# Kernel optimization log

Hardware: AMD Instinct MI355X
Metric: run time of the kernel (lower is better)

The kernel has to match this reference:

```python
import jax, jax.numpy as jnp
import numpy as np
import math

HEADS = 4
LN_EPS = 1e-5


def _layer_norm(x, gamma, beta):
    # LayerNorm over last dim (N=4096), matching nn.LayerNorm(4096)
    mu = jnp.mean(x, axis=-1, keepdims=True)
    var = jnp.mean((x - mu) ** 2, axis=-1, keepdims=True)
    return (x - mu) * jax.lax.rsqrt(var + LN_EPS) * gamma + beta


def setup_inputs() -> dict:
    key = jax.random.key(0)
    ks = jax.random.split(key, 10)
    L, IMG, N = 1024, 1024, 4096
    s_img = 1.0 / math.sqrt(IMG)
    s_L = 1.0 / math.sqrt(L)
    return {
        "point_features": jax.random.normal(ks[0], (1, L, N), jnp.float32),
        "img_features": jax.random.normal(ks[1], (1, IMG, N), jnp.float32),
        # 4 per-head 1x1 convs IMG_chl -> L_chl
        "W_img": jax.random.normal(ks[2], (HEADS, L, IMG), jnp.float32) * s_img,
        "b_img": jax.random.normal(ks[3], (HEADS, L), jnp.float32) * s_img,
        # conv_L: L_chl -> L_chl
        "W_L": jax.random.normal(ks[4], (L, L), jnp.float32) * s_L,
        "b_L": jax.random.normal(ks[5], (L,), jnp.float32) * s_L,
        # LayerNorm(4096)
        "ln_g": jnp.ones((N,), jnp.float32),
        "ln_b": jnp.zeros((N,), jnp.float32),
        # conv_fusion: L_chl -> L_chl
        "W_f": jax.random.normal(ks[6], (L, L), jnp.float32) * s_L,
        "b_f": jax.random.normal(ks[7], (L,), jnp.float32) * s_L,
    }


def reference(point_features, img_features, W_img, b_img, W_L, b_L, ln_g, ln_b, W_f, b_f):
    # L_query = conv_L(point_features): [1, L, N]
    L_query = jnp.einsum('oi,bin->bon', W_L, point_features) + b_L[None, :, None]
    dk = L_query.shape[1]
    N = L_query.shape[2]

    # All 4 head keys at once: [H, 1, L, N]
    keys = jnp.einsum('hoi,bin->hbon', W_img, img_features) + b_img[:, None, :, None]

    # score_i = sum_c(key_i * query) / sqrt(dk)  -> cat over heads: [H, N] (B=1)
    score = jnp.sum(keys * L_query[None], axis=2).reshape(HEADS, N) / jnp.sqrt(jnp.float32(dk))

    # softmax across heads (dim=0), weightmap = [1, H, N]
    weight = jax.nn.softmax(score, axis=0)
    weightmap = weight[None]

    # z = sum_h weight[h] * key_h : [1, L, N]
    z = jnp.einsum('hn,hbcn->bcn', weight, keys)

    fused = _layer_norm(z + L_query, ln_g, ln_b)
    fusion_features = jnp.einsum('oi,bin->bon', W_f, fused) + b_f[None, :, None]
    return (fusion_features, weightmap)
```

## Files before the change

### kernel.cpp

```cpp
#include <hip/hip_runtime.h>
#include <hip/hip_bf16.h>
#include <stdint.h>

using u16 = unsigned short;

typedef __attribute__((ext_vector_type(8))) short bf16x8;
typedef __attribute__((ext_vector_type(4))) float f32x4;

typedef const __attribute__((address_space(1))) unsigned int* gas_t;
typedef __attribute__((address_space(3))) unsigned int* las_t;

__device__ inline void g2l16(const u16* g, u16* l) {
  __builtin_amdgcn_global_load_lds((gas_t)g, (las_t)l, 16, 0, 0);
}

__device__ inline u16 f2b(float x) {
  union { float f; uint32_t u; } v; v.f = x;
  uint32_t r = (v.u + 0x7FFFu + ((v.u >> 16) & 1u)) >> 16;
  return (u16)r;
}
__device__ inline float b2f(u16 b) {
  union { uint32_t u; float f; } v; v.u = ((uint32_t)b) << 16;
  return v.f;
}

__device__ inline void store_out(float* p, float v) { *p = v; }
__device__ inline void store_out(u16* p, float v) { *p = f2b(v); }

template<typename OutT>
__global__ __launch_bounds__(256)
void gemm_bt(const u16* __restrict__ A, const u16* __restrict__ Bt,
             const float* __restrict__ bias, OutT* __restrict__ C,
             int M, int N, int K)
{
  __shared__ u16 As[128 * 64];
  __shared__ u16 Bs[128 * 64];

  const int tid  = threadIdx.x;
  const int wave = tid >> 6;
  const int lane = tid & 63;
  const int wm = wave >> 1, wn = wave & 1;
  const int lr = lane & 15;
  const int lq = lane >> 4;
  const int x7 = lr & 7;

  const int m0 = blockIdx.y * 128;
  const int n0 = blockIdx.x * 128;

  const int srow = tid >> 3;
  const int sgc  = (tid & 7) ^ (srow & 7);
  const u16* gA = A  + (size_t)(m0 + srow) * K + sgc * 8;
  const u16* gB = Bt + (size_t)(n0 + srow) * K + sgc * 8;
  u16* dstA = As + wave * 512;
  u16* dstB = Bs + wave * 512;

  f32x4 acc[4][4];
  #pragma unroll
  for (int i = 0; i < 4; ++i)
    #pragma unroll
    for (int j = 0; j < 4; ++j)
      acc[i][j] = (f32x4){0.f, 0.f, 0.f, 0.f};

  for (int k0 = 0; k0 < K; k0 += 64) {
    #pragma unroll
    for (int s = 0; s < 4; ++s) {
      g2l16(gA + (size_t)(s * 32) * K + k0, dstA + s * 2048);
      g2l16(gB + (size_t)(s * 32) * K + k0, dstB + s * 2048);
    }
    __syncthreads();

    #pragma unroll
    for (int ks = 0; ks < 2; ++ks) {
      const int pa = (ks * 4 + lq) ^ x7;
      bf16x8 af[4], bfr[4];
      #pragma unroll
      for (int im = 0; im < 4; ++im)
        af[im] = *(const bf16x8*)&As[(wm * 64 + im * 16 + lr) * 64 + pa * 8];
      #pragma unroll
      for (int in = 0; in < 4; ++in)
        bfr[in] = *(const bf16x8*)&Bs[(wn * 64 + in * 16 + lr) * 64 + pa * 8];

      #pragma unroll
      for (int im = 0; im < 4; ++im)
        #pragma unroll
        for (int in = 0; in < 4; ++in)
          acc[im][in] = __builtin_amdgcn_mfma_f32_16x16x32_bf16(
              af[im], bfr[in], acc[im][in], 0, 0, 0);
    }
    __syncthreads();
  }

  #pragma unroll
  for (int im = 0; im < 4; ++im) {
    const int mbase = m0 + wm * 64 + im * 16 + lq * 4;
    #pragma unroll
    for (int in = 0; in < 4; ++in) {
      const int ncol = n0 + wn * 64 + in * 16 + lr;
      #pragma unroll
      for (int r = 0; r < 4; ++r) {
        const int m = mbase + r;
        store_out(C + (size_t)m * N + ncol, acc[im][in][r] + bias[m]);
      }
    }
  }
}

template<typename OutT>
__global__ __launch_bounds__(256)
void gemm_bt_64(const u16* __restrict__ A, const u16* __restrict__ Bt,
                const float* __restrict__ bias, OutT* __restrict__ C,
                int M, int N, int K)
{
  __shared__ u16 As[64 * 64];
  __shared__ u16 Bs[128 * 64];

  const int tid  = threadIdx.x;
  const int wave = tid >> 6;
  const int lane = tid & 63;
  const int lr = lane & 15;
  const int lq = lane >> 4;
  const int x7 = lr & 7;

  const int m0 = blockIdx.y * 64;
  const int n0 = blockIdx.x * 128;

  const int srow = tid >> 3;
  const int sgc  = (tid & 7) ^ (srow & 7);
  const u16* gA = A  + (size_t)(m0 + srow) * K + sgc * 8;
  const u16* gB = Bt + (size_t)(n0 + srow) * K + sgc * 8;
  u16* dstA = As + wave * 512;
  u16* dstB = Bs + wave * 512;

  f32x4 acc[4][2];
  #pragma unroll
  for (int i = 0; i < 4; ++i)
    #pragma unroll
    for (int j = 0; j < 2; ++j)
      acc[i][j] = (f32x4){0.f, 0.f, 0.f, 0.f};

  for (int k0 = 0; k0 < K; k0 += 64) {
    #pragma unroll
    for (int s = 0; s < 2; ++s)
      g2l16(gA + (size_t)(s * 32) * K + k0, dstA + s * 2048);
    #pragma unroll
    for (int s = 0; s < 4; ++s)
      g2l16(gB + (size_t)(s * 32) * K + k0, dstB + s * 2048);
    __syncthreads();

    #pragma unroll
    for (int ks = 0; ks < 2; ++ks) {
      const int pa = (ks * 4 + lq) ^ x7;
      bf16x8 af[4], bfr[2];
      #pragma unroll
      for (int im = 0; im < 4; ++im)
        af[im] = *(const bf16x8*)&As[(im * 16 + lr) * 64 + pa * 8];
      #pragma unroll
      for (int in = 0; in < 2; ++in)
        bfr[in] = *(const bf16x8*)&Bs[(wave * 32 + in * 16 + lr) * 64 + pa * 8];

      #pragma unroll
      for (int im = 0; im < 4; ++im)
        #pragma unroll
        for (int in = 0; in < 2; ++in)
          acc[im][in] = __builtin_amdgcn_mfma_f32_16x16x32_bf16(
              af[im], bfr[in], acc[im][in], 0, 0, 0);
    }
    __syncthreads();
  }

  #pragma unroll
  for (int im = 0; im < 4; ++im) {
    const int mbase = m0 + im * 16 + lq * 4;
    #pragma unroll
    for (int in = 0; in < 2; ++in) {
      const int ncol = n0 + wave * 32 + in * 16 + lr;
      #pragma unroll
      for (int r = 0; r < 4; ++r) {
        const int m = mbase + r;
        store_out(C + (size_t)m * N + ncol, acc[im][in][r] + bias[m]);
      }
    }
  }
}

__global__ __launch_bounds__(256)
void cast_transpose2(const float* __restrict__ in0, u16* __restrict__ out0,
                     const float* __restrict__ in1, u16* __restrict__ out1,
                     int R, int C)
{
  const float* in = blockIdx.z ? in1 : in0;
  u16* out = blockIdx.z ? out1 : out0;
  __shared__ u16 tile[32][33];
  const int c0 = blockIdx.x * 32, r0 = blockIdx.y * 32;
  const int tx = threadIdx.x & 31, ty = threadIdx.x >> 5;
  #pragma unroll
  for (int k = 0; k < 4; ++k)
    tile[ty + 8 * k][tx] = f2b(in[(size_t)(r0 + ty + 8 * k) * C + c0 + tx]);
  __syncthreads();
  #pragma unroll
  for (int k = 0; k < 4; ++k)
    out[(size_t)(c0 + ty + 8 * k) * R + r0 + tx] = tile[tx][ty + 8 * k];
}

__global__ __launch_bounds__(256)
void transpose_u16(const u16* __restrict__ in, u16* __restrict__ out,
                   int R, int C)
{
  __shared__ u16 tile[32][33];
  const int c0 = blockIdx.x * 32, r0 = blockIdx.y * 32;
  const int tx = threadIdx.x & 31, ty = threadIdx.x >> 5;
  #pragma unroll
  for (int k = 0; k < 4; ++k)
    tile[ty + 8 * k][tx] = in[(size_t)(r0 + ty + 8 * k) * C + c0 + tx];
  __syncthreads();
  #pragma unroll
  for (int k = 0; k < 4; ++k)
    out[(size_t)(c0 + ty + 8 * k) * R + r0 + tx] = tile[tx][ty + 8 * k];
}

__global__ __launch_bounds__(256)
void cast_weights(const float4* __restrict__ wim, const float4* __restrict__ wl,
                  const float4* __restrict__ wf, ushort4* __restrict__ wimb,
                  ushort4* __restrict__ wlb, ushort4* __restrict__ wfb)
{
  int i = blockIdx.x * 256 + threadIdx.x;
  const float4* src; ushort4* dst;
  if (i < 1048576)      { src = wim; dst = wimb; }
  else if (i < 1310720) { src = wl;  dst = wlb;  i -= 1048576; }
  else                  { src = wf;  dst = wfb;  i -= 1310720; }
  const float4 v = src[i];
  ushort4 o;
  o.x = f2b(v.x); o.y = f2b(v.y); o.z = f2b(v.z); o.w = f2b(v.w);
  dst[i] = o;
}

__global__ __launch_bounds__(256)
void score_partial(const u16* __restrict__ keys, const float* __restrict__ Q,
                   float* __restrict__ spart)
{
  const int n  = blockIdx.x * 256 + threadIdx.x;
  const int cb = blockIdx.y;
  const int c0 = cb * 128;
  float s[4] = {0.f, 0.f, 0.f, 0.f};
  for (int c = c0; c < c0 + 128; ++c) {
    const float q = Q[(size_t)c * 4096 + n];
    #pragma unroll
    for (int h = 0; h < 4; ++h)
      s[h] = fmaf(q, b2f(keys[((size_t)((h << 10) + c)) * 4096 + n]), s[h]);
  }
  #pragma unroll
  for (int h = 0; h < 4; ++h)
    spart[((size_t)cb * 4 + h) * 4096 + n] = s[h];
}

__global__ __launch_bounds__(256)
void softmax_h(const float* __restrict__ spart, float* __restrict__ wmap)
{
  const int n = blockIdx.x * 256 + threadIdx.x;
  float s[4] = {0.f, 0.f, 0.f, 0.f};
  #pragma unroll
  for (int cb = 0; cb < 8; ++cb)
    #pragma unroll
    for (int h = 0; h < 4; ++h)
      s[h] += spart[((size_t)cb * 4 + h) * 4096 + n];
  #pragma unroll
  for (int h = 0; h < 4; ++h) s[h] *= 0.03125f;
  const float m = fmaxf(fmaxf(s[0], s[1]), fmaxf(s[2], s[3]));
  const float e0 = expf(s[0] - m), e1 = expf(s[1] - m);
  const float e2 = expf(s[2] - m), e3 = expf(s[3] - m);
  const float inv = 1.f / (e0 + e1 + e2 + e3);
  wmap[n] = e0 * inv; wmap[4096 + n] = e1 * inv;
  wmap[8192 + n] = e2 * inv; wmap[12288 + n] = e3 * inv;
}

__global__ __launch_bounds__(256)
void z_ln(const u16* __restrict__ keys, const float* __restrict__ Q,
          const float* __restrict__ w, const float* __restrict__ g,
          const float* __restrict__ bb, u16* __restrict__ fused)
{
  const int c  = blockIdx.x;
  const int tx = threadIdx.x;
  float t[16];
  float s = 0.f, s2 = 0.f;
  #pragma unroll
  for (int j = 0; j < 16; ++j) {
    const int n = tx + j * 256;
    const float q = Q[(size_t)c * 4096 + n];
    float z = 0.f;
    #pragma unroll
    for (int h = 0; h < 4; ++h)
      z = fmaf(w[h * 4096 + n], b2f(keys[((size_t)((h << 10) + c)) * 4096 + n]), z);
    const float v = z + q;
    t[j] = v; s += v; s2 = fmaf(v, v, s2);
  }
  #pragma unroll
  for (int o = 32; o > 0; o >>= 1) {
    s  += __shfl_down(s, o);
    s2 += __shfl_down(s2, o);
  }
  __shared__ float rbuf[8];
  const int wave = tx >> 6, lane = tx & 63;
  if (lane == 0) { rbuf[wave] = s; rbuf[4 + wave] = s2; }
  __syncthreads();
  s  = rbuf[0] + rbuf[1] + rbuf[2] + rbuf[3];
  s2 = rbuf[4] + rbuf[5] + rbuf[6] + rbuf[7];
  const float mu  = s * (1.f / 4096.f);
  const float var = s2 * (1.f / 4096.f) - mu * mu;
  const float rs  = rsqrtf(var + 1e-5f);
  #pragma unroll
  for (int j = 0; j < 16; ++j) {
    const int n = tx + j * 256;
    fused[(size_t)c * 4096 + n] = f2b((t[j] - mu) * rs * g[n] + bb[n]);
  }
}

extern "C" void kernel_launch(void* const* d_in, const int* in_sizes, int n_in,
                              void* d_out, int out_size, void* d_ws, size_t ws_size,
                              hipStream_t stream)
{
  const float* P   = (const float*)d_in[0];
  const float* I   = (const float*)d_in[1];
  const float* Wim = (const float*)d_in[2];
  const float* bim = (const float*)d_in[3];
  const float* WL  = (const float*)d_in[4];
  const float* bL  = (const float*)d_in[5];
  const float* lng = (const float*)d_in[6];
  const float* lnb = (const float*)d_in[7];
  const float* Wf  = (const float*)d_in[8];
  const float* bf_ = (const float*)d_in[9];
  float* out = (float*)d_out;

  char* ws = (char*)d_ws;
  u16*   PT     = (u16*)(ws + 0);
  u16*   IT     = (u16*)(ws + (size_t)8  * 1048576);
  u16*   WLb    = (u16*)(ws + (size_t)16 * 1048576);
  u16*   WIb    = (u16*)(ws + (size_t)18 * 1048576);
  u16*   WFb    = (u16*)(ws + (size_t)26 * 1048576);
  float* Q      = (float*)(ws + (size_t)28 * 1048576);
  u16*   KEYS   = (u16*)(ws + (size_t)44 * 1048576);
  float* SPART  = (float*)(ws + (size_t)76 * 1048576);
  u16*   FUSED  = (u16*)(ws + (size_t)77 * 1048576);
  u16*   FUSEDT = (u16*)(ws + (size_t)85 * 1048576);

  const dim3 b256(256);

  cast_transpose2<<<dim3(128, 32, 2), b256, 0, stream>>>(P, PT, I, IT, 1024, 4096);
  cast_weights<<<6144, b256, 0, stream>>>((const float4*)Wim, (const float4*)WL,
                                          (const float4*)Wf, (ushort4*)WIb,
                                          (ushort4*)WLb, (ushort4*)WFb);

  gemm_bt_64<float><<<dim3(32, 16), b256, 0, stream>>>(WLb, PT, bL, Q, 1024, 4096, 1024);
  gemm_bt<u16><<<dim3(32, 32), b256, 0, stream>>>(WIb, IT, bim, KEYS, 4096, 4096, 1024);

  score_partial<<<dim3(16, 8), b256, 0, stream>>>(KEYS, Q, SPART);
  float* wmap = out + (size_t)1024 * 4096;
  softmax_h<<<16, b256, 0, stream>>>(SPART, wmap);

  z_ln<<<1024, b256, 0, stream>>>(KEYS, Q, wmap, lng, lnb, FUSED);
  transpose_u16<<<dim3(128, 32), b256, 0, stream>>>(FUSED, FUSEDT, 1024, 4096);

  gemm_bt_64<float><<<dim3(32, 16), b256, 0, stream>>>(WFb, FUSEDT, bf_, out, 1024, 4096, 1024);
}
```

Measured before the change: 232.0 us.

## Merge prep kernels, fuse Q and keys GEMMs, store Q as bf16

Merges the input cast-transpose and weight-cast kernels into one prep launch. The Q projection and the four-head key projection now run in a single 128x128-tile GEMM launch with 1280 blocks instead of two launches, which removes a launch and a tail. Q is stored as bf16 rather than fp32, halving its write and read traffic in the score and LayerNorm stages. In exchange the residual L_query path loses precision, since it is rounded to bf16.

```diff
diff --git a/kernel.cpp b/kernel.cpp
--- a/kernel.cpp
+++ b/kernel.cpp
@@ -28,14 +28,13 @@
 __device__ inline void store_out(u16* p, float v) { *p = f2b(v); }
 
 template<typename OutT>
-__global__ __launch_bounds__(256)
-void gemm_bt(const u16* __restrict__ A, const u16* __restrict__ Bt,
-             const float* __restrict__ bias, OutT* __restrict__ C,
-             int M, int N, int K)
-{
-  __shared__ u16 As[128 * 64];
-  __shared__ u16 Bs[128 * 64];
-
+__device__ inline void gemm_tile_128(const u16* __restrict__ A,
+                                     const u16* __restrict__ Bt,
+                                     const float* __restrict__ bias,
+                                     OutT* __restrict__ C,
+                                     int m0, int n0, int N, int K,
+                                     u16* As, u16* Bs)
+{
   const int tid  = threadIdx.x;
   const int wave = tid >> 6;
   const int lane = tid & 63;
@@ -44,9 +43,6 @@
   const int lq = lane >> 4;
   const int x7 = lr & 7;
 
-  const int m0 = blockIdx.y * 128;
-  const int n0 = blockIdx.x * 128;
-
   const int srow = tid >> 3;
   const int sgc  = (tid & 7) ^ (srow & 7);
   const u16* gA = A  + (size_t)(m0 + srow) * K + sgc * 8;
@@ -105,6 +101,25 @@
   }
 }
 
+__global__ __launch_bounds__(256)
+void gemm_keys_q(const u16* __restrict__ WIb, const u16* __restrict__ IT,
+                 const float* __restrict__ bim, u16* __restrict__ KEYS,
+                 const u16* __restrict__ WLb, const u16* __restrict__ PT,
+                 const float* __restrict__ bL, u16* __restrict__ Qb)
+{
+  __shared__ u16 As[128 * 64];
+  __shared__ u16 Bs[128 * 64];
+  const int by = blockIdx.y;
+  const bool keys = (by < 32);
+  const u16*   A    = keys ? WIb : WLb;
+  const u16*   Bt   = keys ? IT  : PT;
+  const float* bias = keys ? bim : bL;
+  u16*         C    = keys ? KEYS : Qb;
+  const int m0 = (by & 31) * 128;
+  const int n0 = blockIdx.x * 128;
+  gemm_tile_128<u16>(A, Bt, bias, C, m0, n0, 4096, 1024, As, Bs);
+}
+
 template<typename OutT>
 __global__ __launch_bounds__(256)
 void gemm_bt_64(const u16* __restrict__ A, const u16* __restrict__ Bt,
@@ -184,18 +199,53 @@
 }
 
 __global__ __launch_bounds__(256)
-void cast_transpose2(const float* __restrict__ in0, u16* __restrict__ out0,
-                     const float* __restrict__ in1, u16* __restrict__ out1,
-                     int R, int C)
-{
-  const float* in = blockIdx.z ? in1 : in0;
-  u16* out = blockIdx.z ? out1 : out0;
+void prep(const float* __restrict__ P, u16* __restrict__ PT,
+          const float* __restrict__ I, u16* __restrict__ IT,
+          const float4* __restrict__ wim, const float4* __restrict__ wl,
+          const float4* __restrict__ wf, ushort4* __restrict__ wimb,
+          ushort4* __restrict__ wlb, ushort4* __restrict__ wfb)
+{
+  const int bid = blockIdx.x;
+  if (bid < 8192) {
+    const int z   = bid >> 12;
+    const int rem = bid & 4095;
+    const int bx  = rem & 127;
+    const int byy = rem >> 7;
+    const float* in = z ? I : P;
+    u16* out = z ? IT : PT;
+    __shared__ u16 tile[32][33];
+    const int c0 = bx * 32, r0 = byy * 32;
+    const int tx = threadIdx.x & 31, ty = threadIdx.x >> 5;
+    #pragma unroll
+    for (int k = 0; k < 4; ++k)
+      tile[ty + 8 * k][tx] = f2b(in[(size_t)(r0 + ty + 8 * k) * 4096 + c0 + tx]);
+    __syncthreads();
+    #pragma unroll
+    for (int k = 0; k < 4; ++k)
+      out[(size_t)(c0 + ty + 8 * k) * 1024 + r0 + tx] = tile[tx][ty + 8 * k];
+  } else {
+    int i = (bid - 8192) * 256 + threadIdx.x;
+    const float4* src; ushort4* dst;
+    if (i < 1048576)      { src = wim; dst = wimb; }
+    else if (i < 1310720) { src = wl;  dst = wlb;  i -= 1048576; }
+    else                  { src = wf;  dst = wfb;  i -= 1310720; }
+    const float4 v = src[i];
+    ushort4 o;
+    o.x = f2b(v.x); o.y = f2b(v.y); o.z = f2b(v.z); o.w = f2b(v.w);
+    dst[i] = o;
+  }
+}
+
+__global__ __launch_bounds__(256)
+void transpose_u16(const u16* __restrict__ in, u16* __restrict__ out,
+                   int R, int C)
+{
   __shared__ u16 tile[32][33];
   const int c0 = blockIdx.x * 32, r0 = blockIdx.y * 32;
   const int tx = threadIdx.x & 31, ty = threadIdx.x >> 5;
   #pragma unroll
   for (int k = 0; k < 4; ++k)
-    tile[ty + 8 * k][tx] = f2b(in[(size_t)(r0 + ty + 8 * k) * C + c0 + tx]);
+    tile[ty + 8 * k][tx] = in[(size_t)(r0 + ty + 8 * k) * C + c0 + tx];
   __syncthreads();
   #pragma unroll
   for (int k = 0; k < 4; ++k)
@@ -203,39 +253,7 @@
 }
 
 __global__ __launch_bounds__(256)
-void transpose_u16(const u16* __restrict__ in, u16* __restrict__ out,
-                   int R, int C)
-{
-  __shared__ u16 tile[32][33];
-  const int c0 = blockIdx.x * 32, r0 = blockIdx.y * 32;
-  const int tx = threadIdx.x & 31, ty = threadIdx.x >> 5;
-  #pragma unroll
-  for (int k = 0; k < 4; ++k)
-    tile[ty + 8 * k][tx] = in[(size_t)(r0 + ty + 8 * k) * C + c0 + tx];
-  __syncthreads();
-  #pragma unroll
-  for (int k = 0; k < 4; ++k)
-    out[(size_t)(c0 + ty + 8 * k) * R + r0 + tx] = tile[tx][ty + 8 * k];
-}
-
-__global__ __launch_bounds__(256)
-void cast_weights(const float4* __restrict__ wim, const float4* __restrict__ wl,
-                  const float4* __restrict__ wf, ushort4* __restrict__ wimb,
-                  ushort4* __restrict__ wlb, ushort4* __restrict__ wfb)
-{
-  int i = blockIdx.x * 256 + threadIdx.x;
-  const float4* src; ushort4* dst;
-  if (i < 1048576)      { src = wim; dst = wimb; }
-  else if (i < 1310720) { src = wl;  dst = wlb;  i -= 1048576; }
-  else                  { src = wf;  dst = wfb;  i -= 1310720; }
-  const float4 v = src[i];
-  ushort4 o;
-  o.x = f2b(v.x); o.y = f2b(v.y); o.z = f2b(v.z); o.w = f2b(v.w);
-  dst[i] = o;
-}
-
-__global__ __launch_bounds__(256)
-void score_partial(const u16* __restrict__ keys, const float* __restrict__ Q,
+void score_partial(const u16* __restrict__ keys, const u16* __restrict__ Qb,
                    float* __restrict__ spart)
 {
   const int n  = blockIdx.x * 256 + threadIdx.x;
@@ -243,7 +261,7 @@
   const int c0 = cb * 128;
   float s[4] = {0.f, 0.f, 0.f, 0.f};
   for (int c = c0; c < c0 + 128; ++c) {
-    const float q = Q[(size_t)c * 4096 + n];
+    const float q = b2f(Qb[(size_t)c * 4096 + n]);
     #pragma unroll
     for (int h = 0; h < 4; ++h)
       s[h] = fmaf(q, b2f(keys[((size_t)((h << 10) + c)) * 4096 + n]), s[h]);
@@ -274,7 +292,7 @@
 }
 
 __global__ __launch_bounds__(256)
-void z_ln(const u16* __restrict__ keys, const float* __restrict__ Q,
+void z_ln(const u16* __restrict__ keys, const u16* __restrict__ Qb,
           const float* __restrict__ w, const float* __restrict__ g,
           const float* __restrict__ bb, u16* __restrict__ fused)
 {
@@ -285,7 +303,7 @@
   #pragma unroll
   for (int j = 0; j < 16; ++j) {
     const int n = tx + j * 256;
-    const float q = Q[(size_t)c * 4096 + n];
+    const float q = b2f(Qb[(size_t)c * 4096 + n]);
     float z = 0.f;
     #pragma unroll
     for (int h = 0; h < 4; ++h)
@@ -336,27 +354,27 @@
   u16*   WLb    = (u16*)(ws + (size_t)16 * 1048576);
   u16*   WIb    = (u16*)(ws + (size_t)18 * 1048576);
   u16*   WFb    = (u16*)(ws + (size_t)26 * 1048576);
-  float* Q      = (float*)(ws + (size_t)28 * 1048576);
-  u16*   KEYS   = (u16*)(ws + (size_t)44 * 1048576);
-  float* SPART  = (float*)(ws + (size_t)76 * 1048576);
-  u16*   FUSED  = (u16*)(ws + (size_t)77 * 1048576);
-  u16*   FUSEDT = (u16*)(ws + (size_t)85 * 1048576);
+  u16*   Qb     = (u16*)(ws + (size_t)28 * 1048576);
+  u16*   KEYS   = (u16*)(ws + (size_t)36 * 1048576);
+  float* SPART  = (float*)(ws + (size_t)68 * 1048576);
+  u16*   FUSED  = (u16*)(ws + (size_t)70 * 1048576);
+  u16*   FUSEDT = (u16*)(ws + (size_t)78 * 1048576);
 
   const dim3 b256(256);
 
-  cast_transpose2<<<dim3(128, 32, 2), b256, 0, stream>>>(P, PT, I, IT, 1024, 4096);
-  cast_weights<<<6144, b256, 0, stream>>>((const float4*)Wim, (const float4*)WL,
-                                          (const float4*)Wf, (ushort4*)WIb,
-                                          (ushort4*)WLb, (ushort4*)WFb);
-
-  gemm_bt_64<float><<<dim3(32, 16), b256, 0, stream>>>(WLb, PT, bL, Q, 1024, 4096, 1024);
-  gemm_bt<u16><<<dim3(32, 32), b256, 0, stream>>>(WIb, IT, bim, KEYS, 4096, 4096, 1024);
-
-  score_partial<<<dim3(16, 8), b256, 0, stream>>>(KEYS, Q, SPART);
+  prep<<<14336, b256, 0, stream>>>(P, PT, I, IT,
+                                   (const float4*)Wim, (const float4*)WL,
+                                   (const float4*)Wf, (ushort4*)WIb,
+                                   (ushort4*)WLb, (ushort4*)WFb);
+
+  gemm_keys_q<<<dim3(32, 40), b256, 0, stream>>>(WIb, IT, bim, KEYS,
+                                                 WLb, PT, bL, Qb);
+
+  score_partial<<<dim3(16, 8), b256, 0, stream>>>(KEYS, Qb, SPART);
   float* wmap = out + (size_t)1024 * 4096;
   softmax_h<<<16, b256, 0, stream>>>(SPART, wmap);
 
-  z_ln<<<1024, b256, 0, stream>>>(KEYS, Q, wmap, lng, lnb, FUSED);
+  z_ln<<<1024, b256, 0, stream>>>(KEYS, Qb, wmap, lng, lnb, FUSED);
   transpose_u16<<<dim3(128, 32), b256, 0, stream>>>(FUSED, FUSEDT, 1024, 4096);
 
   gemm_bt_64<float><<<dim3(32, 16), b256, 0, stream>>>(WFb, FUSEDT, bf_, out, 1024, 4096, 1024);
```

After: 219.0 us. -5.6%, faster.
